# Performance work log

Hardware: AMD Instinct MI355X
Metric: run time of the kernel (lower is better)

Reference implementation:

```python
import jax, jax.numpy as jnp
import numpy as np

ALPHA = 0.01  # LeakyReLU negative slope
NEG_INF = -1e12

def setup_inputs() -> dict:
    key = jax.random.key(0)
    k1, k2, k3, k4 = jax.random.split(key, 4)
    B, N, F_in, F_out = 8, 2048, 256, 128
    inp = jax.random.normal(k1, (B, N, F_in), dtype=jnp.float32)
    adj = jax.random.randint(k2, (B, N, N), 0, 2, dtype=jnp.int32)
    # xavier_uniform with gain=1.414
    limW = 1.414 * np.sqrt(6.0 / (F_in + F_out))
    W = jax.random.uniform(k3, (F_in, F_out), minval=-limW, maxval=limW, dtype=jnp.float32)
    lima = 1.414 * np.sqrt(6.0 / (2 * F_out + 1))
    a = jax.random.uniform(k4, (2 * F_out, 1), minval=-lima, maxval=lima, dtype=jnp.float32)
    return {"inp": inp, "adj": adj, "W": W, "a": a}

def reference(inp, adj, W, a):
    # h: [B, N, F_out]
    h = jnp.matmul(inp, W)
    F_out = W.shape[1]
    # Algebraic split of the attention vector: a = [a1; a2], so
    # e[b,i,j] = leakyrelu(h_i . a1 + h_j . a2)  -- avoids the O(N^2*2F) a_input.
    a1 = a[:F_out, 0]   # [F_out]
    a2 = a[F_out:, 0]   # [F_out]
    s1 = jnp.einsum('bnf,f->bn', h, a1)  # [B, N] source term
    s2 = jnp.einsum('bnf,f->bn', h, a2)  # [B, N] target term
    e = s1[:, :, None] + s2[:, None, :]  # [B, N, N]
    e = jnp.where(e > 0, e, ALPHA * e)   # leaky relu
    scores = jnp.where(adj > 0, e, NEG_INF)
    attention = jax.nn.softmax(scores, axis=2)  # [B, N, N]
    h_prime = jnp.matmul(attention, h)          # [B, N, F_out]
    return jax.nn.relu(h_prime)  # concat=True branch
```

## Files before the change

kernel.cpp:

```cpp
#include <hip/hip_runtime.h>
#include <hip/hip_bf16.h>

#define N_    2048
#define FIN   256
#define FOUT  128
#define ALPHA 0.01f

typedef short bf16x8 __attribute__((ext_vector_type(8)));
typedef float f32x4  __attribute__((ext_vector_type(4)));

static __device__ __forceinline__ unsigned short f2bf(float x) {
    __hip_bfloat16 h = __float2bfloat16(x);
    return *reinterpret_cast<unsigned short*>(&h);
}

__global__ __launch_bounds__(256) void k_lin(
    const float* __restrict__ inp, const float* __restrict__ W,
    const float* __restrict__ av, __hip_bfloat16* __restrict__ hT,
    float* __restrict__ s1, float* __restrict__ s2)
{
    __shared__ float in_lds[32 * FIN];
    int g = blockIdx.x;
    int b = g & 7;
    int tile = g >> 3;
    int i0 = tile << 5;
    int t = threadIdx.x;

    const float4* src = reinterpret_cast<const float4*>(inp + ((size_t)(b * N_ + i0)) * FIN);
    float4* dst = reinterpret_cast<float4*>(in_lds);
#pragma unroll
    for (int c = 0; c < 8; ++c) dst[t + 256 * c] = src[t + 256 * c];
    __syncthreads();

    int fq = t & 31;
    int rg = t >> 5;
    float acc[4][4];
#pragma unroll
    for (int r = 0; r < 4; ++r)
#pragma unroll
        for (int j = 0; j < 4; ++j) acc[r][j] = 0.f;

    const float4* W4 = reinterpret_cast<const float4*>(W);
    for (int k = 0; k < FIN; k += 4) {
        float4 inr[4];
#pragma unroll
        for (int r = 0; r < 4; ++r)
            inr[r] = *reinterpret_cast<const float4*>(&in_lds[(rg * 4 + r) * FIN + k]);
#pragma unroll
        for (int kk = 0; kk < 4; ++kk) {
            float4 w4 = W4[(k + kk) * 32 + fq];
#pragma unroll
            for (int r = 0; r < 4; ++r) {
                float iv = (&inr[r].x)[kk];
                acc[r][0] = fmaf(iv, w4.x, acc[r][0]);
                acc[r][1] = fmaf(iv, w4.y, acc[r][1]);
                acc[r][2] = fmaf(iv, w4.z, acc[r][2]);
                acc[r][3] = fmaf(iv, w4.w, acc[r][3]);
            }
        }
    }

    float a1v[4], a2v[4];
#pragma unroll
    for (int j = 0; j < 4; ++j) {
        a1v[j] = av[fq * 4 + j];
        a2v[j] = av[FOUT + fq * 4 + j];
    }
#pragma unroll
    for (int r = 0; r < 4; ++r) {
        float p1 = acc[r][0] * a1v[0] + acc[r][1] * a1v[1] + acc[r][2] * a1v[2] + acc[r][3] * a1v[3];
        float p2 = acc[r][0] * a2v[0] + acc[r][1] * a2v[1] + acc[r][2] * a2v[2] + acc[r][3] * a2v[3];
#pragma unroll
        for (int off = 1; off < 32; off <<= 1) {
            p1 += __shfl_xor(p1, off);
            p2 += __shfl_xor(p2, off);
        }
        if (fq == 0) {
            int row = i0 + rg * 4 + r;
            s1[b * N_ + row] = p1;
            s2[b * N_ + row] = p2;
        }
    }

    __syncthreads();
    unsigned short* hb = reinterpret_cast<unsigned short*>(in_lds);
#pragma unroll
    for (int j = 0; j < 4; ++j)
#pragma unroll
        for (int r = 0; r < 4; ++r)
            hb[(fq * 4 + j) * 33 + rg * 4 + r] = f2bf(acc[r][j]);
    __syncthreads();
    {
        int f = t >> 1;
        int c0 = (t & 1) * 16;
        unsigned short tmp[16];
#pragma unroll
        for (int c = 0; c < 16; ++c) tmp[c] = hb[f * 33 + c0 + c];
        int4* dst4 = reinterpret_cast<int4*>(&hT[((size_t)(b * FOUT + f)) * N_ + i0 + c0]);
        dst4[0] = reinterpret_cast<const int4*>(tmp)[0];
        dst4[1] = reinterpret_cast<const int4*>(tmp)[1];
    }
}

__global__ __launch_bounds__(256) void k_s2max(const float* __restrict__ s2,
                                               float* __restrict__ s2max)
{
    __shared__ float red[4];
    int b = blockIdx.x, t = threadIdx.x;
    const float4* p = reinterpret_cast<const float4*>(s2 + b * N_);
    float4 v0 = p[t], v1 = p[t + 256];
    float m = fmaxf(fmaxf(fmaxf(v0.x, v0.y), fmaxf(v0.z, v0.w)),
                    fmaxf(fmaxf(v1.x, v1.y), fmaxf(v1.z, v1.w)));
#pragma unroll
    for (int off = 1; off < 64; off <<= 1) m = fmaxf(m, __shfl_xor(m, off));
    if ((t & 63) == 0) red[t >> 6] = m;
    __syncthreads();
    if (t == 0) s2max[b] = fmaxf(fmaxf(red[0], red[1]), fmaxf(red[2], red[3]));
}

__global__ __launch_bounds__(256) void k_attn(
    const int* __restrict__ adj, const __hip_bfloat16* __restrict__ hT,
    const float* __restrict__ s1g, const float* __restrict__ s2g,
    const float* __restrict__ s2maxg, float* __restrict__ out)
{
    __shared__ float s2_lds[N_];
    __shared__ float accb[4][16][128];
    __shared__ float l_s[4][16];

    int g = blockIdx.x;
    int b = g & 7;
    int tile = g >> 3;
    int i0 = tile << 4;
    int t = threadIdx.x;
    int w = t >> 6;
    int l = t & 63;
    int r = l & 15;
    int lg = l >> 4;
    int jc = w * 512;

    {
        const float4* s2g4 = reinterpret_cast<const float4*>(s2g + b * N_);
        reinterpret_cast<float4*>(s2_lds)[t] = s2g4[t];
        reinterpret_cast<float4*>(s2_lds)[t + 256] = s2g4[t + 256];
    }

    const float s1r = s1g[b * N_ + i0 + r];
    float eb = s1r + s2maxg[b];
    const float m_row = fmaxf(eb, ALPHA * eb);

    const int4* adjp = reinterpret_cast<const int4*>(
        adj + ((size_t)(b * N_ + i0 + r)) * N_ + jc + lg * 8);
    const bf16x8* hvp = reinterpret_cast<const bf16x8*>(hT)
        + ((((size_t)(b * FOUT + r)) * N_ + jc + lg * 8) >> 3);

    __syncthreads();

    float l_run = 0.0f;
    f32x4 acc[8];
#pragma unroll
    for (int q = 0; q < 8; ++q) acc[q] = (f32x4){0.f, 0.f, 0.f, 0.f};

    int4 ajA0, ajA1, ajB0, ajB1;
    bf16x8 hA[8], hB[8];

    auto pf_hv = [&](bf16x8 (&hd)[8], int S) {
#pragma unroll
        for (int q = 0; q < 8; ++q) hd[q] = hvp[q * 4096 + S * 4];
    };
    auto compute_step = [&](int S, int4 c0, int4 c1, const bf16x8 (&hc)[8]) {
        const float* s2b = &s2_lds[jc + S * 32 + lg * 8];
        float4 ca = *reinterpret_cast<const float4*>(s2b);
        float4 cb = *reinterpret_cast<const float4*>(s2b + 4);
        float sv[8] = {ca.x, ca.y, ca.z, ca.w, cb.x, cb.y, cb.z, cb.w};
        int am[8] = {c0.x, c0.y, c0.z, c0.w, c1.x, c1.y, c1.z, c1.w};
        bf16x8 af;
        float ps = 0.f;
#pragma unroll
        for (int e = 0; e < 8; ++e) {
            float v = s1r + sv[e];
            v = fmaxf(v, ALPHA * v);
            float p = (am[e] > 0) ? __expf(v - m_row) : 0.f;
            ps += p;
            af[e] = (short)f2bf(p);
        }
        l_run += ps;
#pragma unroll
        for (int q = 0; q < 8; ++q)
            acc[q] = __builtin_amdgcn_mfma_f32_16x16x32_bf16(af, hc[q], acc[q], 0, 0, 0);
    };

    ajA0 = adjp[0];  ajA1 = adjp[1];
    ajB0 = adjp[8];  ajB1 = adjp[9];
    pf_hv(hA, 0);

#pragma unroll 1
    for (int it = 0; it < 7; ++it) {
        const int sE = 2 * it;
        {
            int4 c0 = ajA0, c1 = ajA1;
            ajA0 = adjp[(sE + 2) * 8];
            ajA1 = adjp[(sE + 2) * 8 + 1];
            pf_hv(hB, sE + 1);
            compute_step(sE, c0, c1, hA);
        }
        {
            int4 c0 = ajB0, c1 = ajB1;
            ajB0 = adjp[(sE + 3) * 8];
            ajB1 = adjp[(sE + 3) * 8 + 1];
            pf_hv(hA, sE + 2);
            compute_step(sE + 1, c0, c1, hB);
        }
    }
    {
        int4 c0 = ajA0, c1 = ajA1;
        pf_hv(hB, 15);
        compute_step(14, c0, c1, hA);
        compute_step(15, ajB0, ajB1, hB);
    }

    l_run += __shfl_xor(l_run, 16);
    l_run += __shfl_xor(l_run, 32);
    if (l < 16) l_s[w][l] = l_run;

#pragma unroll
    for (int q = 0; q < 8; ++q)
#pragma unroll
        for (int rr = 0; rr < 4; ++rr)
            accb[w][lg * 4 + rr][q * 16 + r] = acc[q][rr];
    __syncthreads();

    int f = t & 127;
    int rh = t >> 7;
#pragma unroll
    for (int rr = 0; rr < 8; ++rr) {
        int row = rh * 8 + rr;
        float L = l_s[0][row] + l_s[1][row] + l_s[2][row] + l_s[3][row];
        float v = accb[0][row][f] + accb[1][row][f] + accb[2][row][f] + accb[3][row][f];
        v = v / L;
        out[((size_t)(b * N_ + i0 + row)) * FOUT + f] = fmaxf(v, 0.f);
    }
}

extern "C" void kernel_launch(void* const* d_in, const int* in_sizes, int n_in,
                              void* d_out, int out_size, void* d_ws, size_t ws_size,
                              hipStream_t stream) {
    (void)in_sizes; (void)n_in; (void)out_size; (void)ws_size;
    const float* inp = (const float*)d_in[0];
    const int*   adj = (const int*)d_in[1];
    const float* W   = (const float*)d_in[2];
    const float* a   = (const float*)d_in[3];
    float* out = (float*)d_out;

    char* ws = (char*)d_ws;
    __hip_bfloat16* hT = (__hip_bfloat16*)ws;
    float* s1 = (float*)(ws + (size_t)8 * FOUT * N_ * 2);
    float* s2 = s1 + 8 * N_;
    float* s2max = s2 + 8 * N_;

    k_lin<<<512, 256, 0, stream>>>(inp, W, a, hT, s1, s2);
    k_s2max<<<8, 256, 0, stream>>>(s2, s2max);
    k_attn<<<1024, 256, 0, stream>>>(adj, hT, s1, s2, s2max, out);
}
```

Measured before the change: 288.2 us.

## Use split-bf16 MFMA for projection and bit-pack adjacency in separate pass

The projection GEMM moves from scalar FP32 FMAs to MFMA using a hi/lo bf16 split (three MFMAs per tile) with a swizzled LDS layout and 64-row tiles. A new kernel packs the int32 adjacency into a bitmask, and the attention kernel reads mask bytes instead of int4 adjacency, with its loop fully unrolled. The adjacency still has to be read once, in full, by the pack kernel, which then writes the mask back out. Two extra kernel launches are added, and the projection's precision now depends on the bf16 split.

After: 289.7 us. No clear change (+0.5%).

```diff
diff --git a/kernel.cpp b/kernel.cpp
--- a/kernel.cpp
+++ b/kernel.cpp
@@ -13,92 +13,151 @@
     __hip_bfloat16 h = __float2bfloat16(x);
     return *reinterpret_cast<unsigned short*>(&h);
 }
+static __device__ __forceinline__ float bf2f(unsigned short u) {
+    return __uint_as_float(((unsigned)u) << 16);
+}
+
+__global__ __launch_bounds__(256) void k_wsplit(
+    const float* __restrict__ W, unsigned short* __restrict__ WThi,
+    unsigned short* __restrict__ WTlo)
+{
+    int idx = blockIdx.x * 256 + threadIdx.x;
+    int k = idx >> 7, n = idx & 127;
+    float w = W[k * 128 + n];
+    unsigned short hi = f2bf(w);
+    unsigned short lo = f2bf(w - bf2f(hi));
+    WThi[n * 256 + k] = hi;
+    WTlo[n * 256 + k] = lo;
+}
+
+__global__ __launch_bounds__(256) void k_pack(
+    const int* __restrict__ adj, unsigned int* __restrict__ mask)
+{
+    __shared__ unsigned char mb[256];
+    int row = blockIdx.x;
+    int t = threadIdx.x;
+    const int4* a4 = reinterpret_cast<const int4*>(adj + (size_t)row * N_) + 2 * t;
+    int4 x = a4[0], y = a4[1];
+    unsigned byte =
+        (unsigned)(x.x > 0) | ((unsigned)(x.y > 0) << 1) |
+        ((unsigned)(x.z > 0) << 2) | ((unsigned)(x.w > 0) << 3) |
+        ((unsigned)(y.x > 0) << 4) | ((unsigned)(y.y > 0) << 5) |
+        ((unsigned)(y.z > 0) << 6) | ((unsigned)(y.w > 0) << 7);
+    int w = t >> 6, cig = t & 63;
+    int S = cig >> 2, lg = cig & 3;
+    mb[w * 64 + lg * 16 + S] = (unsigned char)byte;
+    __syncthreads();
+    if (t < 16)
+        reinterpret_cast<uint4*>(mask)[row * 16 + t] =
+            reinterpret_cast<const uint4*>(mb)[t];
+}
 
 __global__ __launch_bounds__(256) void k_lin(
-    const float* __restrict__ inp, const float* __restrict__ W,
-    const float* __restrict__ av, __hip_bfloat16* __restrict__ hT,
+    const float* __restrict__ inp,
+    const unsigned short* __restrict__ WThi, const unsigned short* __restrict__ WTlo,
+    const float* __restrict__ av, unsigned short* __restrict__ hT,
     float* __restrict__ s1, float* __restrict__ s2)
 {
-    __shared__ float in_lds[32 * FIN];
+    __shared__ unsigned short Ahi[64 * 256];
+    __shared__ unsigned short Alo[64 * 256];
+
     int g = blockIdx.x;
     int b = g & 7;
-    int tile = g >> 3;
-    int i0 = tile << 5;
+    int i0 = (g >> 3) << 6;
     int t = threadIdx.x;
 
-    const float4* src = reinterpret_cast<const float4*>(inp + ((size_t)(b * N_ + i0)) * FIN);
-    float4* dst = reinterpret_cast<float4*>(in_lds);
-#pragma unroll
-    for (int c = 0; c < 8; ++c) dst[t + 256 * c] = src[t + 256 * c];
-    __syncthreads();
-
-    int fq = t & 31;
-    int rg = t >> 5;
-    float acc[4][4];
-#pragma unroll
-    for (int r = 0; r < 4; ++r)
-#pragma unroll
-        for (int j = 0; j < 4; ++j) acc[r][j] = 0.f;
-
-    const float4* W4 = reinterpret_cast<const float4*>(W);
-    for (int k = 0; k < FIN; k += 4) {
-        float4 inr[4];
-#pragma unroll
-        for (int r = 0; r < 4; ++r)
-            inr[r] = *reinterpret_cast<const float4*>(&in_lds[(rg * 4 + r) * FIN + k]);
-#pragma unroll
-        for (int kk = 0; kk < 4; ++kk) {
-            float4 w4 = W4[(k + kk) * 32 + fq];
-#pragma unroll
-            for (int r = 0; r < 4; ++r) {
-                float iv = (&inr[r].x)[kk];
-                acc[r][0] = fmaf(iv, w4.x, acc[r][0]);
-                acc[r][1] = fmaf(iv, w4.y, acc[r][1]);
-                acc[r][2] = fmaf(iv, w4.z, acc[r][2]);
-                acc[r][3] = fmaf(iv, w4.w, acc[r][3]);
+    {
+        int row = t >> 2;
+        const float* src = inp + ((size_t)(b * N_ + i0 + row)) * FIN + (t & 3) * 64;
+#pragma unroll
+        for (int gseg = 0; gseg < 8; ++gseg) {
+            float4 f0 = *reinterpret_cast<const float4*>(src + gseg * 8);
+            float4 f1 = *reinterpret_cast<const float4*>(src + gseg * 8 + 4);
+            float f[8] = {f0.x, f0.y, f0.z, f0.w, f1.x, f1.y, f1.z, f1.w};
+            bf16x8 hi8, lo8;
+#pragma unroll
+            for (int e = 0; e < 8; ++e) {
+                unsigned short h = f2bf(f[e]);
+                hi8[e] = (short)h;
+                lo8[e] = (short)f2bf(f[e] - bf2f(h));
             }
-        }
-    }
-
-    float a1v[4], a2v[4];
-#pragma unroll
-    for (int j = 0; j < 4; ++j) {
-        a1v[j] = av[fq * 4 + j];
-        a2v[j] = av[FOUT + fq * 4 + j];
-    }
-#pragma unroll
-    for (int r = 0; r < 4; ++r) {
-        float p1 = acc[r][0] * a1v[0] + acc[r][1] * a1v[1] + acc[r][2] * a1v[2] + acc[r][3] * a1v[3];
-        float p2 = acc[r][0] * a2v[0] + acc[r][1] * a2v[1] + acc[r][2] * a2v[2] + acc[r][3] * a2v[3];
-#pragma unroll
-        for (int off = 1; off < 32; off <<= 1) {
-            p1 += __shfl_xor(p1, off);
-            p2 += __shfl_xor(p2, off);
-        }
-        if (fq == 0) {
-            int row = i0 + rg * 4 + r;
-            s1[b * N_ + row] = p1;
-            s2[b * N_ + row] = p2;
-        }
-    }
-
-    __syncthreads();
-    unsigned short* hb = reinterpret_cast<unsigned short*>(in_lds);
-#pragma unroll
-    for (int j = 0; j < 4; ++j)
-#pragma unroll
-        for (int r = 0; r < 4; ++r)
-            hb[(fq * 4 + j) * 33 + rg * 4 + r] = f2bf(acc[r][j]);
+            int k = (t & 3) * 64 + gseg * 8;
+            int off = (row * 512 + k * 2) ^ ((row & 7) << 4);
+            *reinterpret_cast<bf16x8*>(reinterpret_cast<char*>(Ahi) + off) = hi8;
+            *reinterpret_cast<bf16x8*>(reinterpret_cast<char*>(Alo) + off) = lo8;
+        }
+    }
+    __syncthreads();
+
+    int w = t >> 6, l = t & 63;
+    int ln = l & 15, lg = l >> 4;
+    const bf16x8* Whi8 = reinterpret_cast<const bf16x8*>(WThi);
+    const bf16x8* Wlo8 = reinterpret_cast<const bf16x8*>(WTlo);
+
+    f32x4 acc[8];
+#pragma unroll
+    for (int nb = 0; nb < 8; ++nb) acc[nb] = (f32x4){0.f, 0.f, 0.f, 0.f};
+
+#pragma unroll
+    for (int ks = 0; ks < 8; ++ks) {
+        int arow = w * 16 + ln;
+        int aoff = (arow * 512 + ks * 64 + lg * 16) ^ ((arow & 7) << 4);
+        bf16x8 ahi = *reinterpret_cast<const bf16x8*>(reinterpret_cast<const char*>(Ahi) + aoff);
+        bf16x8 alo = *reinterpret_cast<const bf16x8*>(reinterpret_cast<const char*>(Alo) + aoff);
+#pragma unroll
+        for (int nb = 0; nb < 8; ++nb) {
+            int n = nb * 16 + ln;
+            bf16x8 whi = Whi8[n * 32 + ks * 4 + lg];
+            bf16x8 wlo = Wlo8[n * 32 + ks * 4 + lg];
+            acc[nb] = __builtin_amdgcn_mfma_f32_16x16x32_bf16(ahi, whi, acc[nb], 0, 0, 0);
+            acc[nb] = __builtin_amdgcn_mfma_f32_16x16x32_bf16(alo, whi, acc[nb], 0, 0, 0);
+            acc[nb] = __builtin_amdgcn_mfma_f32_16x16x32_bf16(ahi, wlo, acc[nb], 0, 0, 0);
+        }
+    }
+
+    float p1[4] = {0.f, 0.f, 0.f, 0.f}, p2[4] = {0.f, 0.f, 0.f, 0.f};
+#pragma unroll
+    for (int nb = 0; nb < 8; ++nb) {
+        float a1 = av[nb * 16 + ln];
+        float a2 = av[FOUT + nb * 16 + ln];
+#pragma unroll
+        for (int j = 0; j < 4; ++j) {
+            p1[j] = fmaf(acc[nb][j], a1, p1[j]);
+            p2[j] = fmaf(acc[nb][j], a2, p2[j]);
+        }
+    }
+#pragma unroll
+    for (int off = 1; off < 16; off <<= 1)
+#pragma unroll
+        for (int j = 0; j < 4; ++j) {
+            p1[j] += __shfl_xor(p1[j], off);
+            p2[j] += __shfl_xor(p2[j], off);
+        }
+    if (ln == 0) {
+#pragma unroll
+        for (int j = 0; j < 4; ++j) {
+            int row = i0 + w * 16 + lg * 4 + j;
+            s1[b * N_ + row] = p1[j];
+            s2[b * N_ + row] = p2[j];
+        }
+    }
+
+    __syncthreads();
+    unsigned short* T = Ahi;
+#pragma unroll
+    for (int nb = 0; nb < 8; ++nb)
+#pragma unroll
+        for (int j = 0; j < 4; ++j)
+            T[(nb * 16 + ln) * 68 + w * 16 + lg * 4 + j] = f2bf(acc[nb][j]);
     __syncthreads();
     {
-        int f = t >> 1;
-        int c0 = (t & 1) * 16;
-        unsigned short tmp[16];
-#pragma unroll
-        for (int c = 0; c < 16; ++c) tmp[c] = hb[f * 33 + c0 + c];
-        int4* dst4 = reinterpret_cast<int4*>(&hT[((size_t)(b * FOUT + f)) * N_ + i0 + c0]);
-        dst4[0] = reinterpret_cast<const int4*>(tmp)[0];
-        dst4[1] = reinterpret_cast<const int4*>(tmp)[1];
+        int f = t & 127, rh = t >> 7;
+        unsigned short tmp[32];
+#pragma unroll
+        for (int c = 0; c < 32; ++c) tmp[c] = T[f * 68 + rh * 32 + c];
+        int4* dst = reinterpret_cast<int4*>(&hT[((size_t)(b * FOUT + f)) * N_ + i0 + rh * 32]);
+#pragma unroll
+        for (int c = 0; c < 4; ++c) dst[c] = reinterpret_cast<const int4*>(tmp)[c];
     }
 }
 
@@ -119,7 +178,7 @@
 }
 
 __global__ __launch_bounds__(256) void k_attn(
-    const int* __restrict__ adj, const __hip_bfloat16* __restrict__ hT,
+    const unsigned int* __restrict__ mask, const unsigned short* __restrict__ hT,
     const float* __restrict__ s1g, const float* __restrict__ s2g,
     const float* __restrict__ s2maxg, float* __restrict__ out)
 {
@@ -129,13 +188,10 @@
 
     int g = blockIdx.x;
     int b = g & 7;
-    int tile = g >> 3;
-    int i0 = tile << 4;
+    int i0 = (g >> 3) << 4;
     int t = threadIdx.x;
-    int w = t >> 6;
-    int l = t & 63;
-    int r = l & 15;
-    int lg = l >> 4;
+    int w = t >> 6, l = t & 63;
+    int r = l & 15, lg = l >> 4;
     int jc = w * 512;
 
     {
@@ -148,8 +204,11 @@
     float eb = s1r + s2maxg[b];
     const float m_row = fmaxf(eb, ALPHA * eb);
 
-    const int4* adjp = reinterpret_cast<const int4*>(
-        adj + ((size_t)(b * N_ + i0 + r)) * N_ + jc + lg * 8);
+    uint4 m4 = *reinterpret_cast<const uint4*>(
+        reinterpret_cast<const char*>(mask) +
+        ((size_t)(b * N_ + i0 + r)) * 256 + w * 64 + lg * 16);
+    unsigned mw[4] = {m4.x, m4.y, m4.z, m4.w};
+
     const bf16x8* hvp = reinterpret_cast<const bf16x8*>(hT)
         + ((((size_t)(b * FOUT + r)) * N_ + jc + lg * 8) >> 3);
 
@@ -160,62 +219,38 @@
 #pragma unroll
     for (int q = 0; q < 8; ++q) acc[q] = (f32x4){0.f, 0.f, 0.f, 0.f};
 
-    int4 ajA0, ajA1, ajB0, ajB1;
-    bf16x8 hA[8], hB[8];
-
-    auto pf_hv = [&](bf16x8 (&hd)[8], int S) {
-#pragma unroll
-        for (int q = 0; q < 8; ++q) hd[q] = hvp[q * 4096 + S * 4];
-    };
-    auto compute_step = [&](int S, int4 c0, int4 c1, const bf16x8 (&hc)[8]) {
+    bf16x8 h0[8], h1[8];
+#pragma unroll
+    for (int q = 0; q < 8; ++q) h0[q] = hvp[q * 4096];
+
+#pragma unroll
+    for (int S = 0; S < 16; ++S) {
+        auto& cur = (S & 1) ? h1 : h0;
+        auto& nxt = (S & 1) ? h0 : h1;
+        if (S < 15) {
+#pragma unroll
+            for (int q = 0; q < 8; ++q) nxt[q] = hvp[q * 4096 + (S + 1) * 4];
+        }
+        unsigned byte = (mw[S >> 2] >> ((S & 3) * 8)) & 0xffu;
         const float* s2b = &s2_lds[jc + S * 32 + lg * 8];
         float4 ca = *reinterpret_cast<const float4*>(s2b);
         float4 cb = *reinterpret_cast<const float4*>(s2b + 4);
         float sv[8] = {ca.x, ca.y, ca.z, ca.w, cb.x, cb.y, cb.z, cb.w};
-        int am[8] = {c0.x, c0.y, c0.z, c0.w, c1.x, c1.y, c1.z, c1.w};
+
         bf16x8 af;
         float ps = 0.f;
 #pragma unroll
         for (int e = 0; e < 8; ++e) {
             float v = s1r + sv[e];
             v = fmaxf(v, ALPHA * v);
-            float p = (am[e] > 0) ? __expf(v - m_row) : 0.f;
+            float p = (byte & (1u << e)) ? __expf(v - m_row) : 0.f;
             ps += p;
             af[e] = (short)f2bf(p);
         }
         l_run += ps;
 #pragma unroll
         for (int q = 0; q < 8; ++q)
-            acc[q] = __builtin_amdgcn_mfma_f32_16x16x32_bf16(af, hc[q], acc[q], 0, 0, 0);
-    };
-
-    ajA0 = adjp[0];  ajA1 = adjp[1];
-    ajB0 = adjp[8];  ajB1 = adjp[9];
-    pf_hv(hA, 0);
-
-#pragma unroll 1
-    for (int it = 0; it < 7; ++it) {
-        const int sE = 2 * it;
-        {
-            int4 c0 = ajA0, c1 = ajA1;
-            ajA0 = adjp[(sE + 2) * 8];
-            ajA1 = adjp[(sE + 2) * 8 + 1];
-            pf_hv(hB, sE + 1);
-            compute_step(sE, c0, c1, hA);
-        }
-        {
-            int4 c0 = ajB0, c1 = ajB1;
-            ajB0 = adjp[(sE + 3) * 8];
-            ajB1 = adjp[(sE + 3) * 8 + 1];
-            pf_hv(hA, sE + 2);
-            compute_step(sE + 1, c0, c1, hB);
-        }
-    }
-    {
-        int4 c0 = ajA0, c1 = ajA1;
-        pf_hv(hB, 15);
-        compute_step(14, c0, c1, hA);
-        compute_step(15, ajB0, ajB1, hB);
+            acc[q] = __builtin_amdgcn_mfma_f32_16x16x32_bf16(af, cur[q], acc[q], 0, 0, 0);
     }
 
     l_run += __shfl_xor(l_run, 16);
@@ -229,15 +264,13 @@
             accb[w][lg * 4 + rr][q * 16 + r] = acc[q][rr];
     __syncthreads();
 
-    int f = t & 127;
-    int rh = t >> 7;
+    int f = t & 127, rh = t >> 7;
 #pragma unroll
     for (int rr = 0; rr < 8; ++rr) {
         int row = rh * 8 + rr;
         float L = l_s[0][row] + l_s[1][row] + l_s[2][row] + l_s[3][row];
         float v = accb[0][row][f] + accb[1][row][f] + accb[2][row][f] + accb[3][row][f];
-        v = v / L;
-        out[((size_t)(b * N_ + i0 + row)) * FOUT + f] = fmaxf(v, 0.f);
+        out[((size_t)(b * N_ + i0 + row)) * FOUT + f] = fmaxf(v / L, 0.f);
     }
 }
 
@@ -252,12 +285,17 @@
     float* out = (float*)d_out;
 
     char* ws = (char*)d_ws;
-    __hip_bfloat16* hT = (__hip_bfloat16*)ws;
-    float* s1 = (float*)(ws + (size_t)8 * FOUT * N_ * 2);
-    float* s2 = s1 + 8 * N_;
-    float* s2max = s2 + 8 * N_;
-
-    k_lin<<<512, 256, 0, stream>>>(inp, W, a, hT, s1, s2);
+    unsigned short* hT   = (unsigned short*)ws;
+    unsigned int*   mask = (unsigned int*)(ws + (4u << 20));
+    float* s1    = (float*)(ws + (8u << 20));
+    float* s2    = s1 + 8 * N_;
+    unsigned short* WThi = (unsigned short*)(s2 + 8 * N_);
+    unsigned short* WTlo = WThi + FIN * FOUT;
+    float* s2max = (float*)(WTlo + FIN * FOUT);
+
+    k_wsplit<<<128, 256, 0, stream>>>(W, WThi, WTlo);
+    k_pack<<<8 * N_, 256, 0, stream>>>(adj, mask);
+    k_lin<<<256, 256, 0, stream>>>(inp, WThi, WTlo, a, hT, s1, s2);
     k_s2max<<<8, 256, 0, stream>>>(s2, s2max);
-    k_attn<<<1024, 256, 0, stream>>>(adj, hT, s1, s2, s2max, out);
-}
+    k_attn<<<1024, 256, 0, stream>>>(mask, hT, s1, s2, s2max, out);
+}
```
